# Optimization experiments

Hardware: AMD Instinct MI355X
Metric: run time of the kernel (lower is better)

## Reference

```python
import jax, jax.numpy as jnp
import numpy as np

RADIUS = 0.2
NSAMPLE = 32
EPS = 1e-5  # BatchNorm2d default eps


def _bn_relu(x, g, b):
    # BatchNorm2d in training mode: per-channel stats over (B, S, nsample), biased var.
    m = x.mean(axis=(0, 1, 2))
    v = jnp.mean((x - m) ** 2, axis=(0, 1, 2))
    return jax.nn.relu((x - m) * jax.lax.rsqrt(v + EPS) * g + b)


def setup_inputs() -> dict:
    key = jax.random.key(0)
    ks = jax.random.split(key, 8)
    B, N, S = 8, 8192, 2048
    xyz = jax.random.uniform(ks[0], (B, 3, N), dtype=jnp.float32)          # unit cube
    points = jax.random.normal(ks[1], (B, 3, N), dtype=jnp.float32)
    fps_idx = jax.random.randint(ks[2], (B, S), 0, N, dtype=jnp.int32)
    W1 = jax.random.normal(ks[3], (64, 6), dtype=jnp.float32) * 0.1
    W2 = jax.random.normal(ks[4], (64, 64), dtype=jnp.float32) * 0.1
    W3 = jax.random.normal(ks[5], (128, 64), dtype=jnp.float32) * 0.1
    return dict(
        xyz=xyz, points=points, fps_idx=fps_idx,
        W1=W1, g1=jnp.ones((64,)), b1=jnp.zeros((64,)),
        W2=W2, g2=jnp.ones((64,)), b2=jnp.zeros((64,)),
        W3=W3, g3=jnp.ones((128,)), b3=jnp.zeros((128,)),
    )


def reference(xyz, points, fps_idx, W1, g1, b1, W2, g2, b2, W3, g3, b3):
    B, _, N = xyz.shape
    xyz_t = jnp.transpose(xyz, (0, 2, 1))            # [B,N,3]
    pts_t = jnp.transpose(points, (0, 2, 1))         # [B,N,D]
    # gather_operation: sampled centers
    new_xyz_t = jnp.take_along_axis(xyz_t, fps_idx[:, :, None], axis=1)  # [B,S,3]
    # ball query: first NSAMPLE points within radius; pad with first hit
    d2 = jnp.sum((new_xyz_t[:, :, None, :] - xyz_t[:, None, :, :]) ** 2, axis=-1)  # [B,S,N]
    keys = jnp.where(d2 <= RADIUS * RADIUS, jnp.arange(N, dtype=jnp.int32), N)
    neg_top, _ = jax.lax.top_k(-keys, NSAMPLE)       # smallest keys first
    idx = -neg_top                                   # [B,S,NSAMPLE]
    idx = jnp.where(idx < N, idx, idx[:, :, 0:1])    # pad empty slots with first hit (self always in-radius)
    bidx = jnp.arange(B)[:, None, None]
    grouped_xyz = xyz_t[bidx, idx]                   # [B,S,ns,3]
    rel = grouped_xyz - new_xyz_t[:, :, None, :]     # center-relative coords
    grouped_pts = pts_t[bidx, idx]                   # [B,S,ns,D]
    feat = jnp.concatenate([rel, grouped_pts], axis=-1)  # [B,S,ns,3+D]
    for W, g, b in ((W1, g1, b1), (W2, g2, b2), (W3, g3, b3)):
        feat = _bn_relu(jnp.einsum('bsnc,oc->bsno', feat, W), g, b)
    new_points = jnp.max(feat, axis=2)               # max over neighbors -> [B,S,C]
    return jnp.transpose(new_xyz_t, (0, 2, 1)), jnp.transpose(new_points, (0, 2, 1))
```

## Files before the change

kernel.cpp:

```cpp
#include <hip/hip_runtime.h>
#include <hip/hip_bf16.h>

#define BB_ 8
#define NN_ 8192
#define SS_ 2048
#define NS 32
#define C1 64
#define C2 64
#define C3 128
#define RAD2 0.04f
#define BN_EPS 1e-5f
#define M_TOT (BB_*SS_*NS)
#define INV_M (1.0f/524288.0f)
#define YSTR 34

typedef __attribute__((ext_vector_type(8))) short bf16x8;
typedef __attribute__((ext_vector_type(4))) float f32x4;

#define FBF_OFF 0
#define WPK_OFF 2097152
#define ST_OFF  2104320
#define GMM_OFF 2104832

__device__ inline unsigned pkbf(float a, float b) {
    __hip_bfloat162 h = __float22bfloat162_rn(make_float2(a, b));
    unsigned r; __builtin_memcpy(&r, &h, 4); return r;
}
__device__ inline bf16x8 asfrag(uint4 v) { bf16x8 r; __builtin_memcpy(&r, &v, 16); return r; }
__device__ inline float bflo(unsigned u) { unsigned x = u << 16; float f; __builtin_memcpy(&f, &x, 4); return f; }
__device__ inline float bfhi(unsigned u) { unsigned x = u & 0xffff0000u; float f; __builtin_memcpy(&f, &x, 4); return f; }

__device__ inline void fin1_ch(const float* __restrict__ st, const float* __restrict__ W1,
                               const float* __restrict__ g, const float* __restrict__ bb,
                               int o, float* __restrict__ al, float* __restrict__ cl) {
    float w[6];
    #pragma unroll
    for (int i = 0; i < 6; ++i) w[i] = W1[o * 6 + i];
    float ms = 0.f;
    #pragma unroll
    for (int i = 0; i < 6; ++i) ms = fmaf(w[i], st[i], ms);
    float m = ms * INV_M;
    float e2 = 0.f;
    #pragma unroll
    for (int ci = 0; ci < 6; ++ci)
        #pragma unroll
        for (int d = 0; d < 6; ++d) {
            int lo = ci < d ? ci : d, hi = ci < d ? d : ci;
            int idx = 6 + lo * 6 - lo * (lo + 1) / 2 + hi;
            e2 = fmaf(w[ci] * w[d], st[idx], e2);
        }
    float var = e2 * INV_M - m * m;
    float ai = g[o] * (1.0f / sqrtf(var + BN_EPS));
    al[o] = ai;
    cl[o] = bb[o] - m * ai;
}

__device__ inline void fin_ch(const float* __restrict__ sum, const float* __restrict__ sq,
                              const float* __restrict__ g, const float* __restrict__ bb,
                              int o, float* __restrict__ al, float* __restrict__ cl) {
    float m = sum[o] * INV_M;
    float var = sq[o] * INV_M - m * m;
    float ai = g[o] * (1.0f / sqrtf(var + BN_EPS));
    al[o] = ai;
    cl[o] = bb[o] - m * ai;
}

__global__ void k_ballquery(const float* __restrict__ xyz, const float* __restrict__ pts,
                            const int* __restrict__ fps, uint4* __restrict__ fbf) {
    __shared__ int lidx[4][NS];
    int wave = (blockIdx.x * blockDim.x + threadIdx.x) >> 6;
    int lane = threadIdx.x & 63;
    int wslot = threadIdx.x >> 6;
    int b = wave / SS_;
    const float* xb = xyz + (size_t)b * 3 * NN_;
    const float* pb = pts + (size_t)b * 3 * NN_;
    int ci = fps[wave];
    float cx = xb[ci], cy = xb[NN_ + ci], cz = xb[2 * NN_ + ci];

    int found = 0;
    int first_i = -1;
    for (int base = 0; base < NN_; base += 64) {
        int i = base + lane;
        float dx = xb[i] - cx, dy = xb[NN_ + i] - cy, dz = xb[2 * NN_ + i] - cz;
        float d2 = __fadd_rn(__fadd_rn(__fmul_rn(dx, dx), __fmul_rn(dy, dy)), __fmul_rn(dz, dz));
        bool inr = d2 <= RAD2;
        unsigned long long mask = __ballot(inr);
        if (first_i < 0 && mask) first_i = base + __builtin_ctzll(mask);
        if (inr) {
            int pos = found + __popcll(mask & ((1ull << lane) - 1ull));
            if (pos < NS) lidx[wslot][pos] = i;
        }
        found += __popcll(mask);
        if (found >= NS) break;
    }
    if (found > NS) found = NS;
    __syncthreads();

    if (lane < NS) {
        int j = (lane < found) ? lidx[wslot][lane] : first_i;
        uint4 o;
        o.x = pkbf(xb[j] - cx,           xb[NN_ + j] - cy);
        o.y = pkbf(xb[2 * NN_ + j] - cz, pb[j]);
        o.z = pkbf(pb[NN_ + j],          pb[2 * NN_ + j]);
        o.w = 0u;
        fbf[(size_t)wave * NS + lane] = o;
    }
}

__global__ void k_pack(const float* __restrict__ W1, const float* __restrict__ W2,
                       const float* __restrict__ W3, uint4* __restrict__ wf,
                       float* __restrict__ st) {
    if (blockIdx.x == 7) { st[threadIdx.x] = 0.f; st[threadIdx.x + 256] = 0.f; return; }
    int t = blockIdx.x * 256 + threadIdx.x;
    int l = t & 63, p = l & 15, qd = l >> 4;
    float v[8];
    if (t < 256) {
        int mt = t >> 6;
        #pragma unroll
        for (int j = 0; j < 8; ++j)
            v[j] = (qd == 0 && j < 6) ? W1[(mt * 16 + p) * 6 + j] : 0.f;
    } else if (t < 768) {
        int fr = (t - 256) >> 6;
        int mt = fr >> 1, kf = fr & 1;
        #pragma unroll
        for (int j = 0; j < 8; ++j)
            v[j] = W2[(16 * mt + p) * 64 + kf * 32 + qd * 8 + j];
    } else {
        int fr = (t - 768) >> 6;
        int nt = fr >> 1, kf = fr & 1;
        #pragma unroll
        for (int j = 0; j < 8; ++j)
            v[j] = W3[(nt * 16 + p) * 64 + kf * 32 + qd * 8 + j];
    }
    uint4 o;
    o.x = pkbf(v[0], v[1]); o.y = pkbf(v[2], v[3]);
    o.z = pkbf(v[4], v[5]); o.w = pkbf(v[6], v[7]);
    wf[t] = o;
}

__global__ void k_p1(const uint4* __restrict__ fbf, float* __restrict__ st) {
    __shared__ float sacc[27];
    int tid = threadIdx.x;
    if (tid < 27) sacc[tid] = 0.f;
    __syncthreads();
    int gt = blockIdx.x * 256 + tid;
    float vals[27];
    #pragma unroll
    for (int i = 0; i < 27; ++i) vals[i] = 0.f;
    #pragma unroll 1
    for (int it = 0; it < M_TOT / 65536; ++it) {
        uint4 w = fbf[it * 65536 + gt];
        float f[6] = { bflo(w.x), bfhi(w.x), bflo(w.y), bfhi(w.y), bflo(w.z), bfhi(w.z) };
        #pragma unroll
        for (int c = 0; c < 6; ++c) vals[c] += f[c];
        int q = 6;
        #pragma unroll
        for (int c = 0; c < 6; ++c)
            #pragma unroll
            for (int d = c; d < 6; ++d) { vals[q] = fmaf(f[c], f[d], vals[q]); ++q; }
    }
    int lane = tid & 63;
    #pragma unroll
    for (int i = 0; i < 27; ++i) {
        float v = vals[i];
        #pragma unroll
        for (int d = 32; d; d >>= 1) v += __shfl_xor(v, d);
        if (lane == 0) atomicAdd(&sacc[i], v);
    }
    __syncthreads();
    if (tid < 27) atomicAdd(&st[tid], sacc[tid]);
}

__global__ __launch_bounds__(256) void k_p2(
        const uint4* __restrict__ fbf, const uint4* __restrict__ wpk,
        float* __restrict__ st,
        const float* __restrict__ W1, const float* __restrict__ g1, const float* __restrict__ b1) {
    __shared__ unsigned yls[4][64 * YSTR];
    __shared__ float bs[C2], bq[C2];
    __shared__ float a1ls[C1], c1ls[C1];
    int tid = threadIdx.x, wslot = tid >> 6, lane = tid & 63;
    int p = lane & 15, qd = lane >> 4;
    if (tid < C2) { bs[tid] = 0.f; bq[tid] = 0.f; }
    if (tid >= 64 && tid < 128) fin1_ch(st, W1, g1, b1, tid - 64, a1ls, c1ls);
    __syncthreads();
    const uint4* w1f = wpk;
    const uint4* w2f = wpk + 256;
    unsigned* my = yls[wslot];
    float s2[4][4], q2[4][4];
    #pragma unroll
    for (int i = 0; i < 4; ++i)
        #pragma unroll
        for (int r = 0; r < 4; ++r) { s2[i][r] = 0.f; q2[i][r] = 0.f; }

    #pragma unroll 1
    for (int it = 0; it < 2; ++it) {
        int tile = it * 4096 + blockIdx.x * 4 + wslot;
        int base = tile * 64;
        bf16x8 B1[4];
        #pragma unroll
        for (int nt = 0; nt < 4; ++nt) {
            uint4 v = make_uint4(0u, 0u, 0u, 0u);
            if (qd == 0) v = fbf[base + nt * 16 + p];
            B1[nt] = asfrag(v);
        }
        #pragma unroll
        for (int mt = 0; mt < 4; ++mt) {
            bf16x8 A = asfrag(w1f[mt * 64 + lane]);
            float4 av = *(const float4*)(a1ls + mt * 16 + qd * 4);
            float4 cv = *(const float4*)(c1ls + mt * 16 + qd * 4);
            #pragma unroll
            for (int nt = 0; nt < 4; ++nt) {
                f32x4 acc = {0.f, 0.f, 0.f, 0.f};
                acc = __builtin_amdgcn_mfma_f32_16x16x32_bf16(A, B1[nt], acc, 0, 0, 0);
                float y0 = fmaxf(fmaf(av.x, acc[0], cv.x), 0.f);
                float y1 = fmaxf(fmaf(av.y, acc[1], cv.y), 0.f);
                float y2 = fmaxf(fmaf(av.z, acc[2], cv.z), 0.f);
                float y3 = fmaxf(fmaf(av.w, acc[3], cv.w), 0.f);
                int a = (nt * 16 + p) * YSTR + mt * 8 + qd * 2;
                *(uint2*)&my[a] = make_uint2(pkbf(y0, y1), pkbf(y2, y3));
            }
        }
        __threadfence_block();
        bf16x8 B2[4][2];
        #pragma unroll
        for (int nt = 0; nt < 4; ++nt)
            #pragma unroll
            for (int kf = 0; kf < 2; ++kf)
                B2[nt][kf] = asfrag(*(const uint4*)&my[(nt * 16 + p) * YSTR + kf * 16 + qd * 4]);
        #pragma unroll
        for (int mt = 0; mt < 4; ++mt) {
            f32x4 acc[4];
            #pragma unroll
            for (int nt = 0; nt < 4; ++nt) acc[nt] = (f32x4){0.f, 0.f, 0.f, 0.f};
            #pragma unroll
            for (int kf = 0; kf < 2; ++kf) {
                bf16x8 W = asfrag(w2f[(mt * 2 + kf) * 64 + lane]);
                #pragma unroll
                for (int nt = 0; nt < 4; ++nt)
                    acc[nt] = __builtin_amdgcn_mfma_f32_16x16x32_bf16(W, B2[nt][kf], acc[nt], 0, 0, 0);
            }
            #pragma unroll
            for (int r = 0; r < 4; ++r) {
                float v0 = acc[0][r], v1 = acc[1][r], v2 = acc[2][r], v3 = acc[3][r];
                s2[mt][r] += (v0 + v1) + (v2 + v3);
                q2[mt][r] = fmaf(v0, v0, fmaf(v1, v1, fmaf(v2, v2, fmaf(v3, v3, q2[mt][r]))));
            }
        }
        __threadfence_block();
    }
    #pragma unroll
    for (int mt = 0; mt < 4; ++mt)
        #pragma unroll
        for (int r = 0; r < 4; ++r) {
            float s = s2[mt][r], q = q2[mt][r];
            #pragma unroll
            for (int off = 1; off <= 8; off <<= 1) { s += __shfl_xor(s, off); q += __shfl_xor(q, off); }
            if (p == 0) {
                atomicAdd(&bs[mt * 16 + qd * 4 + r], s);
                atomicAdd(&bq[mt * 16 + qd * 4 + r], q);
            }
        }
    __syncthreads();
    if (tid < C2) { atomicAdd(&st[64 + tid], bs[tid]); atomicAdd(&st[128 + tid], bq[tid]); }
}

__global__ __launch_bounds__(256) void k_p3(
        const uint4* __restrict__ fbf, const uint4* __restrict__ wpk,
        float* __restrict__ st,
        const float* __restrict__ W1, const float* __restrict__ g1, const float* __restrict__ b1,
        const float* __restrict__ g2, const float* __restrict__ b2,
        const float* __restrict__ g3, float* __restrict__ gmm) {
    __shared__ unsigned yls[4][64 * YSTR];
    __shared__ uint4 w3ls[1024];
    __shared__ float bs[C3], bq[C3];
    __shared__ float a1ls[C1], c1ls[C1], a2ls[C2], c2ls[C2];
    int tid = threadIdx.x, wslot = tid >> 6, lane = tid & 63;
    int p = lane & 15, qd = lane >> 4;
    if (tid < 128) bs[tid] = 0.f; else bq[tid - 128] = 0.f;
    #pragma unroll
    for (int i = 0; i < 4; ++i) w3ls[i * 256 + tid] = wpk[768 + i * 256 + tid];
    if (tid < 64) fin1_ch(st, W1, g1, b1, tid, a1ls, c1ls);
    else if (tid < 128) fin_ch(st + 64, st + 128, g2, b2, tid - 64, a2ls, c2ls);
    __syncthreads();
    const uint4* w1f = wpk;
    const uint4* w2f = wpk + 256;
    unsigned* my = yls[wslot];
    float gs3[8], gq3[8];
    bool pos[8];
    #pragma unroll
    for (int i = 0; i < 8; ++i) { gs3[i] = 0.f; gq3[i] = 0.f; pos[i] = g3[i * 16 + p] >= 0.f; }

    #pragma unroll 1
    for (int it = 0; it < 2; ++it) {
        int tile = it * 4096 + blockIdx.x * 4 + wslot;
        int base = tile * 64;
        bf16x8 B1[4];
        #pragma unroll
        for (int nt = 0; nt < 4; ++nt) {
            uint4 v = make_uint4(0u, 0u, 0u, 0u);
            if (qd == 0) v = fbf[base + nt * 16 + p];
            B1[nt] = asfrag(v);
        }
        #pragma unroll
        for (int mt = 0; mt < 4; ++mt) {
            bf16x8 A = asfrag(w1f[mt * 64 + lane]);
            float4 av = *(const float4*)(a1ls + mt * 16 + qd * 4);
            float4 cv = *(const float4*)(c1ls + mt * 16 + qd * 4);
            #pragma unroll
            for (int nt = 0; nt < 4; ++nt) {
                f32x4 acc = {0.f, 0.f, 0.f, 0.f};
                acc = __builtin_amdgcn_mfma_f32_16x16x32_bf16(A, B1[nt], acc, 0, 0, 0);
                float y0 = fmaxf(fmaf(av.x, acc[0], cv.x), 0.f);
                float y1 = fmaxf(fmaf(av.y, acc[1], cv.y), 0.f);
                float y2 = fmaxf(fmaf(av.z, acc[2], cv.z), 0.f);
                float y3 = fmaxf(fmaf(av.w, acc[3], cv.w), 0.f);
                int a = (nt * 16 + p) * YSTR + mt * 8 + qd * 2;
                *(uint2*)&my[a] = make_uint2(pkbf(y0, y1), pkbf(y2, y3));
            }
        }
        __threadfence_block();
        bf16x8 B2[4][2];
        #pragma unroll
        for (int nt = 0; nt < 4; ++nt)
            #pragma unroll
            for (int kf = 0; kf < 2; ++kf)
                B2[nt][kf] = asfrag(*(const uint4*)&my[(nt * 16 + p) * YSTR + kf * 16 + qd * 4]);
        __threadfence_block();
        #pragma unroll
        for (int mt = 0; mt < 4; ++mt) {
            f32x4 acc[4];
            #pragma unroll
            for (int nt = 0; nt < 4; ++nt) acc[nt] = (f32x4){0.f, 0.f, 0.f, 0.f};
            #pragma unroll
            for (int kf = 0; kf < 2; ++kf) {
                bf16x8 W = asfrag(w2f[(mt * 2 + kf) * 64 + lane]);
                #pragma unroll
                for (int nt = 0; nt < 4; ++nt)
                    acc[nt] = __builtin_amdgcn_mfma_f32_16x16x32_bf16(W, B2[nt][kf], acc[nt], 0, 0, 0);
            }
            float4 av = *(const float4*)(a2ls + mt * 16 + qd * 4);
            float4 cv = *(const float4*)(c2ls + mt * 16 + qd * 4);
            #pragma unroll
            for (int nt = 0; nt < 4; ++nt) {
                float y0 = fmaxf(fmaf(av.x, acc[nt][0], cv.x), 0.f);
                float y1 = fmaxf(fmaf(av.y, acc[nt][1], cv.y), 0.f);
                float y2 = fmaxf(fmaf(av.z, acc[nt][2], cv.z), 0.f);
                float y3 = fmaxf(fmaf(av.w, acc[nt][3], cv.w), 0.f);
                int a = (nt * 16 + p) * YSTR + mt * 8 + qd * 2;
                *(uint2*)&my[a] = make_uint2(pkbf(y0, y1), pkbf(y2, y3));
            }
        }
        __threadfence_block();
        bf16x8 A3[4][2];
        #pragma unroll
        for (int mt = 0; mt < 4; ++mt) {
            A3[mt][0] = asfrag(*(const uint4*)&my[(mt * 16 + p) * YSTR + qd * 4]);
            A3[mt][1] = asfrag(*(const uint4*)&my[(mt * 16 + p) * YSTR + 16 + qd * 4]);
        }
        __threadfence_block();
        #pragma unroll
        for (int nt = 0; nt < 8; ++nt) {
            bf16x8 Wa = asfrag(w3ls[(nt * 2 + 0) * 64 + lane]);
            bf16x8 Wb = asfrag(w3ls[(nt * 2 + 1) * 64 + lane]);
            f32x4 acc[4];
            #pragma unroll
            for (int mt = 0; mt < 4; ++mt) {
                acc[mt] = __builtin_amdgcn_mfma_f32_16x16x32_bf16(A3[mt][0], Wa,
                            (f32x4){0.f, 0.f, 0.f, 0.f}, 0, 0, 0);
                acc[mt] = __builtin_amdgcn_mfma_f32_16x16x32_bf16(A3[mt][1], Wb, acc[mt], 0, 0, 0);
            }
            float s = 0.f, q = 0.f, va = 0.f, vb = 0.f;
            #pragma unroll
            for (int mt = 0; mt < 4; ++mt) {
                float v0 = acc[mt][0], v1 = acc[mt][1], v2 = acc[mt][2], v3 = acc[mt][3];
                s += (v0 + v1) + (v2 + v3);
                q = fmaf(v0, v0, fmaf(v1, v1, fmaf(v2, v2, fmaf(v3, v3, q))));
                float mx = fmaxf(fmaxf(v0, v1), fmaxf(v2, v3));
                float mn = fminf(fminf(v0, v1), fminf(v2, v3));
                float vv = pos[nt] ? mx : -mn;
                if (mt == 0) va = vv;
                else if (mt == 1) va = fmaxf(va, vv);
                else if (mt == 2) vb = vv;
                else vb = fmaxf(vb, vv);
            }
            gs3[nt] += s; gq3[nt] += q;
            va = fmaxf(va, __shfl_xor(va, 16)); va = fmaxf(va, __shfl_xor(va, 32));
            vb = fmaxf(vb, __shfl_xor(vb, 16)); vb = fmaxf(vb, __shfl_xor(vb, 32));
            if (lane < 16) {
                gmm[(size_t)(tile * 2 + 0) * C3 + nt * 16 + lane] = va;
                gmm[(size_t)(tile * 2 + 1) * C3 + nt * 16 + lane] = vb;
            }
        }
    }
    #pragma unroll
    for (int nt = 0; nt < 8; ++nt) {
        float s = gs3[nt], q = gq3[nt];
        s += __shfl_xor(s, 16); s += __shfl_xor(s, 32);
        q += __shfl_xor(q, 16); q += __shfl_xor(q, 32);
        if (lane < 16) {
            atomicAdd(&bs[nt * 16 + lane], s);
            atomicAdd(&bq[nt * 16 + lane], q);
        }
    }
    __syncthreads();
    if (tid < C3) { atomicAdd(&st[192 + tid], bs[tid]); atomicAdd(&st[320 + tid], bq[tid]); }
}

__global__ void k_outx(const float* __restrict__ gmm, const float* __restrict__ st,
                       const float* __restrict__ g3, const float* __restrict__ b3,
                       const float* __restrict__ xyz, const int* __restrict__ fps,
                       float* __restrict__ out) {
    __shared__ float T[C3][17];
    __shared__ float a3ls[C3], c3ls[C3];
    int blk = blockIdx.x, tid = threadIdx.x;
    if (blk < 1024) {
        if (tid < C3) fin_ch(st + 192, st + 320, g3, b3, tid, a3ls, c3ls);
        __syncthreads();
        int b = blk >> 7, s0 = (blk & 127) << 4;
        #pragma unroll
        for (int i = 0; i < 8; ++i) {
            int idx = i * 256 + tid;
            int sl = idx >> 7, o = idx & 127;
            float m = gmm[((size_t)(b * SS_ + s0 + sl)) * C3 + o];
            float a = a3ls[o];
            float v = (a >= 0.f) ? m : -m;
            T[o][sl] = fmaxf(fmaf(a, v, c3ls[o]), 0.f);
        }
        __syncthreads();
        int o = tid & 127, sh = tid >> 7;
        float* dst = out + (size_t)BB_ * 3 * SS_ + ((size_t)b * C3 + o) * SS_ + s0 + sh * 8;
        float4 w0, w1;
        w0.x = T[o][sh * 8 + 0]; w0.y = T[o][sh * 8 + 1];
        w0.z = T[o][sh * 8 + 2]; w0.w = T[o][sh * 8 + 3];
        w1.x = T[o][sh * 8 + 4]; w1.y = T[o][sh * 8 + 5];
        w1.z = T[o][sh * 8 + 6]; w1.w = T[o][sh * 8 + 7];
        *(float4*)dst = w0; *(float4*)(dst + 4) = w1;
    } else {
        int t = (blk - 1024) * 256 + tid;
        int b = t / (3 * SS_);
        int r = (t / SS_) % 3;
        int s = t % SS_;
        int ci = fps[b * SS_ + s];
        out[t] = xyz[((size_t)b * 3 + r) * NN_ + ci];
    }
}

extern "C" void kernel_launch(void* const* d_in, const int* in_sizes, int n_in,
                              void* d_out, int out_size, void* d_ws, size_t ws_size,
                              hipStream_t stream) {
    (void)in_sizes; (void)n_in; (void)out_size; (void)ws_size;
    const float* xyz = (const float*)d_in[0];
    const float* pts = (const float*)d_in[1];
    const int*   fps = (const int*)d_in[2];
    const float* W1 = (const float*)d_in[3];
    const float* g1 = (const float*)d_in[4];
    const float* b1 = (const float*)d_in[5];
    const float* W2 = (const float*)d_in[6];
    const float* g2 = (const float*)d_in[7];
    const float* b2 = (const float*)d_in[8];
    const float* W3 = (const float*)d_in[9];
    const float* g3 = (const float*)d_in[10];
    const float* b3 = (const float*)d_in[11];
    float* out = (float*)d_out;
    float* ws = (float*)d_ws;

    uint4* fbf = (uint4*)(ws + FBF_OFF);
    uint4* wpk = (uint4*)(ws + WPK_OFF);
    float* st  = ws + ST_OFF;
    float* gmm = ws + GMM_OFF;

    k_pack<<<8, 256, 0, stream>>>(W1, W2, W3, wpk, st);
    k_ballquery<<<(BB_ * SS_) / 4, 256, 0, stream>>>(xyz, pts, fps, fbf);
    k_p1<<<256, 256, 0, stream>>>(fbf, st);
    k_p2<<<1024, 256, 0, stream>>>(fbf, wpk, st, W1, g1, b1);
    k_p3<<<1024, 256, 0, stream>>>(fbf, wpk, st, W1, g1, b1, g2, b2, g3, gmm);
    k_outx<<<1024 + 192, 256, 0, stream>>>(gmm, st, g3, b3, xyz, fps, out);
}
```

Baseline: 246.7 us.

## Fuse first-layer input statistics into ball query and drop block fences

Removes the separate k_p1 kernel, which reread the packed bf16 grouped features to accumulate the 27 first and second moments for layer-1 BatchNorm. Those moments are now computed in k_ballquery from the fp32 values while they are still in registers, reduced with wave shuffles and shared/global atomics. It also deletes several __threadfence_block calls in k_p2/k_p3 around per-wave LDS reuse. The moments now come from fp32 rather than bf16-rounded values, so they differ slightly from what the MFMA path consumes. Ball query adds 16384 blocks doing 27 atomics each to the same global addresses, and dropping the fences may allow LDS write/read reordering within a wave.

```diff
diff --git a/kernel.cpp b/kernel.cpp
--- a/kernel.cpp
+++ b/kernel.cpp
@@ -27,8 +27,6 @@
     unsigned r; __builtin_memcpy(&r, &h, 4); return r;
 }
 __device__ inline bf16x8 asfrag(uint4 v) { bf16x8 r; __builtin_memcpy(&r, &v, 16); return r; }
-__device__ inline float bflo(unsigned u) { unsigned x = u << 16; float f; __builtin_memcpy(&f, &x, 4); return f; }
-__device__ inline float bfhi(unsigned u) { unsigned x = u & 0xffff0000u; float f; __builtin_memcpy(&f, &x, 4); return f; }
 
 __device__ inline void fin1_ch(const float* __restrict__ st, const float* __restrict__ W1,
                                const float* __restrict__ g, const float* __restrict__ bb,
@@ -66,11 +64,15 @@
 }
 
 __global__ void k_ballquery(const float* __restrict__ xyz, const float* __restrict__ pts,
-                            const int* __restrict__ fps, uint4* __restrict__ fbf) {
+                            const int* __restrict__ fps, uint4* __restrict__ fbf,
+                            float* __restrict__ st) {
     __shared__ int lidx[4][NS];
-    int wave = (blockIdx.x * blockDim.x + threadIdx.x) >> 6;
-    int lane = threadIdx.x & 63;
-    int wslot = threadIdx.x >> 6;
+    __shared__ float sacc[27];
+    int tid = threadIdx.x;
+    int wave = (blockIdx.x * blockDim.x + tid) >> 6;
+    int lane = tid & 63;
+    int wslot = tid >> 6;
+    if (tid < 27) sacc[tid] = 0.f;
     int b = wave / SS_;
     const float* xb = xyz + (size_t)b * 3 * NN_;
     const float* pb = pts + (size_t)b * 3 * NN_;
@@ -96,15 +98,37 @@
     if (found > NS) found = NS;
     __syncthreads();
 
+    int j = (lane < found && lane < NS) ? lidx[wslot][lane] : first_i;
+    float f[6];
+    f[0] = xb[j] - cx; f[1] = xb[NN_ + j] - cy; f[2] = xb[2 * NN_ + j] - cz;
+    f[3] = pb[j];      f[4] = pb[NN_ + j];      f[5] = pb[2 * NN_ + j];
     if (lane < NS) {
-        int j = (lane < found) ? lidx[wslot][lane] : first_i;
         uint4 o;
-        o.x = pkbf(xb[j] - cx,           xb[NN_ + j] - cy);
-        o.y = pkbf(xb[2 * NN_ + j] - cz, pb[j]);
-        o.z = pkbf(pb[NN_ + j],          pb[2 * NN_ + j]);
-        o.w = 0u;
+        o.x = pkbf(f[0], f[1]); o.y = pkbf(f[2], f[3]); o.z = pkbf(f[4], f[5]); o.w = 0u;
         fbf[(size_t)wave * NS + lane] = o;
-    }
+    } else {
+        #pragma unroll
+        for (int c = 0; c < 6; ++c) f[c] = 0.f;
+    }
+    float vals[27];
+    #pragma unroll
+    for (int c = 0; c < 6; ++c) vals[c] = f[c];
+    {
+        int q = 6;
+        #pragma unroll
+        for (int c = 0; c < 6; ++c)
+            #pragma unroll
+            for (int d = c; d < 6; ++d) { vals[q] = f[c] * f[d]; ++q; }
+    }
+    #pragma unroll
+    for (int i = 0; i < 27; ++i) {
+        float v = vals[i];
+        #pragma unroll
+        for (int d = 32; d; d >>= 1) v += __shfl_xor(v, d);
+        if (lane == 0) atomicAdd(&sacc[i], v);
+    }
+    __syncthreads();
+    if (tid < 27) atomicAdd(&st[tid], sacc[tid]);
 }
 
 __global__ void k_pack(const float* __restrict__ W1, const float* __restrict__ W2,
@@ -136,39 +160,6 @@
     o.x = pkbf(v[0], v[1]); o.y = pkbf(v[2], v[3]);
     o.z = pkbf(v[4], v[5]); o.w = pkbf(v[6], v[7]);
     wf[t] = o;
-}
-
-__global__ void k_p1(const uint4* __restrict__ fbf, float* __restrict__ st) {
-    __shared__ float sacc[27];
-    int tid = threadIdx.x;
-    if (tid < 27) sacc[tid] = 0.f;
-    __syncthreads();
-    int gt = blockIdx.x * 256 + tid;
-    float vals[27];
-    #pragma unroll
-    for (int i = 0; i < 27; ++i) vals[i] = 0.f;
-    #pragma unroll 1
-    for (int it = 0; it < M_TOT / 65536; ++it) {
-        uint4 w = fbf[it * 65536 + gt];
-        float f[6] = { bflo(w.x), bfhi(w.x), bflo(w.y), bfhi(w.y), bflo(w.z), bfhi(w.z) };
-        #pragma unroll
-        for (int c = 0; c < 6; ++c) vals[c] += f[c];
-        int q = 6;
-        #pragma unroll
-        for (int c = 0; c < 6; ++c)
-            #pragma unroll
-            for (int d = c; d < 6; ++d) { vals[q] = fmaf(f[c], f[d], vals[q]); ++q; }
-    }
-    int lane = tid & 63;
-    #pragma unroll
-    for (int i = 0; i < 27; ++i) {
-        float v = vals[i];
-        #pragma unroll
-        for (int d = 32; d; d >>= 1) v += __shfl_xor(v, d);
-        if (lane == 0) atomicAdd(&sacc[i], v);
-    }
-    __syncthreads();
-    if (tid < 27) atomicAdd(&st[tid], sacc[tid]);
 }
 
 __global__ __launch_bounds__(256) void k_p2(
@@ -220,7 +211,6 @@
                 *(uint2*)&my[a] = make_uint2(pkbf(y0, y1), pkbf(y2, y3));
             }
         }
-        __threadfence_block();
         bf16x8 B2[4][2];
         #pragma unroll
         for (int nt = 0; nt < 4; ++nt)
@@ -246,7 +236,6 @@
                 q2[mt][r] = fmaf(v0, v0, fmaf(v1, v1, fmaf(v2, v2, fmaf(v3, v3, q2[mt][r]))));
             }
         }
-        __threadfence_block();
     }
     #pragma unroll
     for (int mt = 0; mt < 4; ++mt)
@@ -318,14 +307,12 @@
                 *(uint2*)&my[a] = make_uint2(pkbf(y0, y1), pkbf(y2, y3));
             }
         }
-        __threadfence_block();
         bf16x8 B2[4][2];
         #pragma unroll
         for (int nt = 0; nt < 4; ++nt)
             #pragma unroll
             for (int kf = 0; kf < 2; ++kf)
                 B2[nt][kf] = asfrag(*(const uint4*)&my[(nt * 16 + p) * YSTR + kf * 16 + qd * 4]);
-        __threadfence_block();
         #pragma unroll
         for (int mt = 0; mt < 4; ++mt) {
             f32x4 acc[4];
@@ -350,14 +337,12 @@
                 *(uint2*)&my[a] = make_uint2(pkbf(y0, y1), pkbf(y2, y3));
             }
         }
-        __threadfence_block();
         bf16x8 A3[4][2];
         #pragma unroll
         for (int mt = 0; mt < 4; ++mt) {
             A3[mt][0] = asfrag(*(const uint4*)&my[(mt * 16 + p) * YSTR + qd * 4]);
             A3[mt][1] = asfrag(*(const uint4*)&my[(mt * 16 + p) * YSTR + 16 + qd * 4]);
         }
-        __threadfence_block();
         #pragma unroll
         for (int nt = 0; nt < 8; ++nt) {
             bf16x8 Wa = asfrag(w3ls[(nt * 2 + 0) * 64 + lane]);
@@ -470,8 +455,7 @@
     float* gmm = ws + GMM_OFF;
 
     k_pack<<<8, 256, 0, stream>>>(W1, W2, W3, wpk, st);
-    k_ballquery<<<(BB_ * SS_) / 4, 256, 0, stream>>>(xyz, pts, fps, fbf);
-    k_p1<<<256, 256, 0, stream>>>(fbf, st);
+    k_ballquery<<<(BB_ * SS_) / 4, 256, 0, stream>>>(xyz, pts, fps, fbf, st);
     k_p2<<<1024, 256, 0, stream>>>(fbf, wpk, st, W1, g1, b1);
     k_p3<<<1024, 256, 0, stream>>>(fbf, wpk, st, W1, g1, b1, g2, b2, g3, gmm);
     k_outx<<<1024 + 192, 256, 0, stream>>>(gmm, st, g3, b3, xyz, fps, out);
```

After: 277.8 us. 1.13x slower.

## Store layer-2 pre-activations in k_p2 and skip recomputing layers 1-2 in p3

Applied to the files above, without the earlier changes.

k_p2 now writes the layer-2 pre-BN outputs as bf16 to a workspace buffer. A new k_p3_l3 reads that buffer, applies BN2+ReLU and computes only layer 3 and the max-pool, so layers 1 and 2 are no longer recomputed. The fused path stays as a fallback when the workspace is too small. k_p2 also moves to 128-thread blocks with four iterations, ball query prefetches the next point chunk, and several fences become __syncthreads. This trades extra global traffic (about 64 MB written and read back) for the removed MFMA recompute.

```diff
diff --git a/kernel.cpp b/kernel.cpp
--- a/kernel.cpp
+++ b/kernel.cpp
@@ -21,6 +21,8 @@
 #define WPK_OFF 2097152
 #define ST_OFF  2104320
 #define GMM_OFF 2104832
+#define X2_OFF  4201984
+#define WS_NEED ((size_t)(4201984 + 16777216) * 4)
 
 __device__ inline unsigned pkbf(float a, float b) {
     __hip_bfloat162 h = __float22bfloat162_rn(make_float2(a, b));
@@ -68,34 +70,36 @@
 __global__ void k_ballquery(const float* __restrict__ xyz, const float* __restrict__ pts,
                             const int* __restrict__ fps, uint4* __restrict__ fbf) {
     __shared__ int lidx[4][NS];
-    int wave = (blockIdx.x * blockDim.x + threadIdx.x) >> 6;
-    int lane = threadIdx.x & 63;
-    int wslot = threadIdx.x >> 6;
+    int tid = threadIdx.x;
+    int wave = (blockIdx.x * blockDim.x + tid) >> 6;
+    int lane = tid & 63;
+    int wslot = tid >> 6;
     int b = wave / SS_;
     const float* xb = xyz + (size_t)b * 3 * NN_;
     const float* pb = pts + (size_t)b * 3 * NN_;
     int ci = fps[wave];
     float cx = xb[ci], cy = xb[NN_ + ci], cz = xb[2 * NN_ + ci];
 
+    float px = xb[lane], py = xb[NN_ + lane], pz = xb[2 * NN_ + lane];
     int found = 0;
     int first_i = -1;
     for (int base = 0; base < NN_; base += 64) {
-        int i = base + lane;
-        float dx = xb[i] - cx, dy = xb[NN_ + i] - cy, dz = xb[2 * NN_ + i] - cz;
+        float xv = px, yv = py, zv = pz;
+        int nb = (base + 64 < NN_) ? base + 64 : 0;
+        px = xb[nb + lane]; py = xb[NN_ + nb + lane]; pz = xb[2 * NN_ + nb + lane];
+        float dx = xv - cx, dy = yv - cy, dz = zv - cz;
         float d2 = __fadd_rn(__fadd_rn(__fmul_rn(dx, dx), __fmul_rn(dy, dy)), __fmul_rn(dz, dz));
         bool inr = d2 <= RAD2;
         unsigned long long mask = __ballot(inr);
         if (first_i < 0 && mask) first_i = base + __builtin_ctzll(mask);
         if (inr) {
             int pos = found + __popcll(mask & ((1ull << lane) - 1ull));
-            if (pos < NS) lidx[wslot][pos] = i;
+            if (pos < NS) lidx[wslot][pos] = base + lane;
         }
         found += __popcll(mask);
         if (found >= NS) break;
     }
     if (found > NS) found = NS;
-    __syncthreads();
-
     if (lane < NS) {
         int j = (lane < found) ? lidx[wslot][lane] : first_i;
         uint4 o;
@@ -171,17 +175,17 @@
     if (tid < 27) atomicAdd(&st[tid], sacc[tid]);
 }
 
-__global__ __launch_bounds__(256) void k_p2(
+__global__ __launch_bounds__(128) void k_p2(
         const uint4* __restrict__ fbf, const uint4* __restrict__ wpk,
         float* __restrict__ st,
-        const float* __restrict__ W1, const float* __restrict__ g1, const float* __restrict__ b1) {
-    __shared__ unsigned yls[4][64 * YSTR];
+        const float* __restrict__ W1, const float* __restrict__ g1, const float* __restrict__ b1,
+        uint2* __restrict__ x2, int store_x2) {
+    __shared__ unsigned yls[2][64 * YSTR];
     __shared__ float bs[C2], bq[C2];
     __shared__ float a1ls[C1], c1ls[C1];
     int tid = threadIdx.x, wslot = tid >> 6, lane = tid & 63;
     int p = lane & 15, qd = lane >> 4;
-    if (tid < C2) { bs[tid] = 0.f; bq[tid] = 0.f; }
-    if (tid >= 64 && tid < 128) fin1_ch(st, W1, g1, b1, tid - 64, a1ls, c1ls);
+    if (tid < C2) { bs[tid] = 0.f; bq[tid] = 0.f; fin1_ch(st, W1, g1, b1, tid, a1ls, c1ls); }
     __syncthreads();
     const uint4* w1f = wpk;
     const uint4* w2f = wpk + 256;
@@ -193,8 +197,8 @@
         for (int r = 0; r < 4; ++r) { s2[i][r] = 0.f; q2[i][r] = 0.f; }
 
     #pragma unroll 1
-    for (int it = 0; it < 2; ++it) {
-        int tile = it * 4096 + blockIdx.x * 4 + wslot;
+    for (int it = 0; it < 4; ++it) {
+        int tile = it * 2048 + blockIdx.x * 2 + wslot;
         int base = tile * 64;
         bf16x8 B1[4];
         #pragma unroll
@@ -220,7 +224,7 @@
                 *(uint2*)&my[a] = make_uint2(pkbf(y0, y1), pkbf(y2, y3));
             }
         }
-        __threadfence_block();
+        __syncthreads();
         bf16x8 B2[4][2];
         #pragma unroll
         for (int nt = 0; nt < 4; ++nt)
@@ -239,14 +243,20 @@
                 for (int nt = 0; nt < 4; ++nt)
                     acc[nt] = __builtin_amdgcn_mfma_f32_16x16x32_bf16(W, B2[nt][kf], acc[nt], 0, 0, 0);
             }
+            if (store_x2) {
+                #pragma unroll
+                for (int nt = 0; nt < 4; ++nt)
+                    x2[(size_t)(tile * 64 + nt * 16 + p) * 16 + mt * 4 + qd] =
+                        make_uint2(pkbf(acc[nt][0], acc[nt][1]), pkbf(acc[nt][2], acc[nt][3]));
+            }
             #pragma unroll
             for (int r = 0; r < 4; ++r) {
-                float v0 = acc[0][r], v1 = acc[1][r], v2 = acc[2][r], v3 = acc[3][r];
-                s2[mt][r] += (v0 + v1) + (v2 + v3);
-                q2[mt][r] = fmaf(v0, v0, fmaf(v1, v1, fmaf(v2, v2, fmaf(v3, v3, q2[mt][r]))));
-            }
-        }
-        __threadfence_block();
+                float u0 = acc[0][r], u1 = acc[1][r], u2 = acc[2][r], u3 = acc[3][r];
+                s2[mt][r] += (u0 + u1) + (u2 + u3);
+                q2[mt][r] = fmaf(u0, u0, fmaf(u1, u1, fmaf(u2, u2, fmaf(u3, u3, q2[mt][r]))));
+            }
+        }
+        __syncthreads();
     }
     #pragma unroll
     for (int mt = 0; mt < 4; ++mt)
@@ -264,7 +274,106 @@
     if (tid < C2) { atomicAdd(&st[64 + tid], bs[tid]); atomicAdd(&st[128 + tid], bq[tid]); }
 }
 
-__global__ __launch_bounds__(256) void k_p3(
+__global__ __launch_bounds__(256) void k_p3_l3(
+        const uint2* __restrict__ x2, const uint4* __restrict__ wpk,
+        float* __restrict__ st,
+        const float* __restrict__ g2, const float* __restrict__ b2,
+        const float* __restrict__ g3, float* __restrict__ gmm) {
+    __shared__ uint4 w3ls[1024];
+    __shared__ float bs[C3], bq[C3];
+    __shared__ float a2ls[C2], c2ls[C2];
+    int tid = threadIdx.x, wslot = tid >> 6, lane = tid & 63;
+    int p = lane & 15, qd = lane >> 4;
+    if (tid < 128) bs[tid] = 0.f; else bq[tid - 128] = 0.f;
+    #pragma unroll
+    for (int i = 0; i < 4; ++i) w3ls[i * 256 + tid] = wpk[768 + i * 256 + tid];
+    if (tid < C2) fin_ch(st + 64, st + 128, g2, b2, tid, a2ls, c2ls);
+    __syncthreads();
+    const uint4* x2u4 = (const uint4*)x2;
+    float a2r[2][8], c2r[2][8];
+    #pragma unroll
+    for (int kf = 0; kf < 2; ++kf)
+        #pragma unroll
+        for (int j = 0; j < 8; ++j) {
+            a2r[kf][j] = a2ls[kf * 32 + qd * 8 + j];
+            c2r[kf][j] = c2ls[kf * 32 + qd * 8 + j];
+        }
+    float gs3[8], gq3[8];
+    bool pos[8];
+    #pragma unroll
+    for (int i = 0; i < 8; ++i) { gs3[i] = 0.f; gq3[i] = 0.f; pos[i] = g3[i * 16 + p] >= 0.f; }
+
+    #pragma unroll 1
+    for (int it = 0; it < 2; ++it) {
+        int tile = it * 4096 + blockIdx.x * 4 + wslot;
+        bf16x8 A3[4][2];
+        #pragma unroll
+        for (int mt = 0; mt < 4; ++mt)
+            #pragma unroll
+            for (int kf = 0; kf < 2; ++kf) {
+                uint4 u = x2u4[(size_t)(tile * 64 + mt * 16 + p) * 8 + kf * 4 + qd];
+                unsigned w[4] = { u.x, u.y, u.z, u.w };
+                unsigned res[4];
+                #pragma unroll
+                for (int wi = 0; wi < 4; ++wi) {
+                    float lo = bflo(w[wi]), hi = bfhi(w[wi]);
+                    float ylo = fmaxf(fmaf(a2r[kf][2 * wi], lo, c2r[kf][2 * wi]), 0.f);
+                    float yhi = fmaxf(fmaf(a2r[kf][2 * wi + 1], hi, c2r[kf][2 * wi + 1]), 0.f);
+                    res[wi] = pkbf(ylo, yhi);
+                }
+                uint4 o;
+                o.x = res[0]; o.y = res[1]; o.z = res[2]; o.w = res[3];
+                A3[mt][kf] = asfrag(o);
+            }
+        #pragma unroll
+        for (int nt = 0; nt < 8; ++nt) {
+            bf16x8 Wa = asfrag(w3ls[(nt * 2 + 0) * 64 + lane]);
+            bf16x8 Wb = asfrag(w3ls[(nt * 2 + 1) * 64 + lane]);
+            f32x4 acc[4];
+            #pragma unroll
+            for (int mt = 0; mt < 4; ++mt) {
+                acc[mt] = __builtin_amdgcn_mfma_f32_16x16x32_bf16(A3[mt][0], Wa,
+                            (f32x4){0.f, 0.f, 0.f, 0.f}, 0, 0, 0);
+                acc[mt] = __builtin_amdgcn_mfma_f32_16x16x32_bf16(A3[mt][1], Wb, acc[mt], 0, 0, 0);
+            }
+            float s = 0.f, q = 0.f, va = 0.f, vb = 0.f;
+            #pragma unroll
+            for (int mt = 0; mt < 4; ++mt) {
+                float v0 = acc[mt][0], v1 = acc[mt][1], v2 = acc[mt][2], v3 = acc[mt][3];
+                s += (v0 + v1) + (v2 + v3);
+                q = fmaf(v0, v0, fmaf(v1, v1, fmaf(v2, v2, fmaf(v3, v3, q))));
+                float mx = fmaxf(fmaxf(v0, v1), fmaxf(v2, v3));
+                float mn = fminf(fminf(v0, v1), fminf(v2, v3));
+                float vv = pos[nt] ? mx : -mn;
+                if (mt == 0) va = vv;
+                else if (mt == 1) va = fmaxf(va, vv);
+                else if (mt == 2) vb = vv;
+                else vb = fmaxf(vb, vv);
+            }
+            gs3[nt] += s; gq3[nt] += q;
+            va = fmaxf(va, __shfl_xor(va, 16)); va = fmaxf(va, __shfl_xor(va, 32));
+            vb = fmaxf(vb, __shfl_xor(vb, 16)); vb = fmaxf(vb, __shfl_xor(vb, 32));
+            if (lane < 16) {
+                gmm[(size_t)(tile * 2 + 0) * C3 + nt * 16 + lane] = va;
+                gmm[(size_t)(tile * 2 + 1) * C3 + nt * 16 + lane] = vb;
+            }
+        }
+    }
+    #pragma unroll
+    for (int nt = 0; nt < 8; ++nt) {
+        float s = gs3[nt], q = gq3[nt];
+        s += __shfl_xor(s, 16); s += __shfl_xor(s, 32);
+        q += __shfl_xor(q, 16); q += __shfl_xor(q, 32);
+        if (lane < 16) {
+            atomicAdd(&bs[nt * 16 + lane], s);
+            atomicAdd(&bq[nt * 16 + lane], q);
+        }
+    }
+    __syncthreads();
+    if (tid < C3) { atomicAdd(&st[192 + tid], bs[tid]); atomicAdd(&st[320 + tid], bq[tid]); }
+}
+
+__global__ __launch_bounds__(256) void k_p3_fused(
         const uint4* __restrict__ fbf, const uint4* __restrict__ wpk,
         float* __restrict__ st,
         const float* __restrict__ W1, const float* __restrict__ g1, const float* __restrict__ b1,
@@ -318,14 +427,14 @@
                 *(uint2*)&my[a] = make_uint2(pkbf(y0, y1), pkbf(y2, y3));
             }
         }
-        __threadfence_block();
+        __syncthreads();
         bf16x8 B2[4][2];
         #pragma unroll
         for (int nt = 0; nt < 4; ++nt)
             #pragma unroll
             for (int kf = 0; kf < 2; ++kf)
                 B2[nt][kf] = asfrag(*(const uint4*)&my[(nt * 16 + p) * YSTR + kf * 16 + qd * 4]);
-        __threadfence_block();
+        __syncthreads();
         #pragma unroll
         for (int mt = 0; mt < 4; ++mt) {
             f32x4 acc[4];
@@ -350,14 +459,14 @@
                 *(uint2*)&my[a] = make_uint2(pkbf(y0, y1), pkbf(y2, y3));
             }
         }
-        __threadfence_block();
+        __syncthreads();
         bf16x8 A3[4][2];
         #pragma unroll
         for (int mt = 0; mt < 4; ++mt) {
             A3[mt][0] = asfrag(*(const uint4*)&my[(mt * 16 + p) * YSTR + qd * 4]);
             A3[mt][1] = asfrag(*(const uint4*)&my[(mt * 16 + p) * YSTR + 16 + qd * 4]);
         }
-        __threadfence_block();
+        __syncthreads();
         #pragma unroll
         for (int nt = 0; nt < 8; ++nt) {
             bf16x8 Wa = asfrag(w3ls[(nt * 2 + 0) * 64 + lane]);
@@ -448,7 +557,7 @@
 extern "C" void kernel_launch(void* const* d_in, const int* in_sizes, int n_in,
                               void* d_out, int out_size, void* d_ws, size_t ws_size,
                               hipStream_t stream) {
-    (void)in_sizes; (void)n_in; (void)out_size; (void)ws_size;
+    (void)in_sizes; (void)n_in; (void)out_size;
     const float* xyz = (const float*)d_in[0];
     const float* pts = (const float*)d_in[1];
     const int*   fps = (const int*)d_in[2];
@@ -468,11 +577,16 @@
     uint4* wpk = (uint4*)(ws + WPK_OFF);
     float* st  = ws + ST_OFF;
     float* gmm = ws + GMM_OFF;
+    uint2* x2  = (uint2*)(ws + X2_OFF);
+    int split = (ws_size >= WS_NEED) ? 1 : 0;
 
     k_pack<<<8, 256, 0, stream>>>(W1, W2, W3, wpk, st);
     k_ballquery<<<(BB_ * SS_) / 4, 256, 0, stream>>>(xyz, pts, fps, fbf);
     k_p1<<<256, 256, 0, stream>>>(fbf, st);
-    k_p2<<<1024, 256, 0, stream>>>(fbf, wpk, st, W1, g1, b1);
-    k_p3<<<1024, 256, 0, stream>>>(fbf, wpk, st, W1, g1, b1, g2, b2, g3, gmm);
+    k_p2<<<1024, 128, 0, stream>>>(fbf, wpk, st, W1, g1, b1, x2, split);
+    if (split)
+        k_p3_l3<<<1024, 256, 0, stream>>>(x2, wpk, st, g2, b2, g3, gmm);
+    else
+        k_p3_fused<<<1024, 256, 0, stream>>>(fbf, wpk, st, W1, g1, b1, g2, b2, g3, gmm);
     k_outx<<<1024 + 192, 256, 0, stream>>>(gmm, st, g3, b3, xyz, fps, out);
 }
```

After: 232.9 us. -5.6%, faster.
